# Kernel optimization log

Measured on AMD Instinct MI355X. Metric: run time of the kernel, lower is better.

The kernel has to match this reference:

```python
import jax, jax.numpy as jnp
import numpy as np

TRUNK = 128  # hard-coded trunk_size in the Triton kernels


def setup_inputs() -> dict:
    key = jax.random.key(0)
    kq, kk, kv = jax.random.split(key, 3)
    N, D = 262144, 64
    Q = jax.random.normal(kq, (N, D), dtype=jnp.float32)
    K = jax.random.normal(kk, (N, D), dtype=jnp.float32)
    V = jax.random.normal(kv, (N, D), dtype=jnp.float32)
    return {"Q": Q, "K": K, "V": V}


def reference(Q, K, V):
    # Faithful to the Triton module:
    # 1) intra kernel overwrites Q in-place with, per trunk t:
    #      Q_t <- Q_t @ (V_t^T K_t)^T = Q_t @ K_t^T @ V_t
    # 2) inter kernel accumulates global state S = sum_t V_t^T K_t = V^T K (fp32)
    # 3) final output = Q_intra @ S
    N, D = Q.shape
    dtype = Q.dtype
    assert N % TRUNK == 0
    T = N // TRUNK
    Qt = Q.reshape(T, TRUNK, D)
    Kt = K.reshape(T, TRUNK, D)
    Vt = V.reshape(T, TRUNK, D)
    # per-trunk scores [T, TRUNK, TRUNK], then apply to V
    scores = jnp.einsum('tnd,tmd->tnm', Qt, Kt)
    Q_intra = jnp.einsum('tnm,tmd->tnd', scores, Vt).reshape(N, D)
    # global DxD state in float32 (atomic_add accumulator dtype)
    S = jnp.einsum('nd,ne->de', V.astype(jnp.float32), K.astype(jnp.float32))
    out = Q_intra @ S.astype(dtype)
    return out
```

## Files before the change

kernel.cpp:

```cpp
#include <hip/hip_runtime.h>
#include <hip/hip_bf16.h>


#define TRUNK 128
#define DD 64
#define NPART 512

typedef __bf16 bf16x8 __attribute__((ext_vector_type(8)));
typedef float  f32x4  __attribute__((ext_vector_type(4)));
typedef unsigned int   u32;
typedef unsigned short u16;
typedef u32 u32x4 __attribute__((ext_vector_type(4)));
typedef u32 u32x2 __attribute__((ext_vector_type(2)));

union F8 { bf16x8 v; u16 u[8]; u32x4 q; };

__device__ __forceinline__ u16 f2bf(float x) {
    union { float f; u32 u; } a; a.f = x;
    u32 u = a.u;
    return (u16)((u + 0x7FFFu + ((u >> 16) & 1u)) >> 16);
}
__device__ __forceinline__ u32 pack2(float a, float b) {
    return (u32)f2bf(a) | ((u32)f2bf(b) << 16);
}

#define P_S  72
#define KV_T 136

__device__ __forceinline__ void stage_T(const float* __restrict__ M, long tb,
                                        u16* __restrict__ MT, int t) {
    #pragma unroll
    for (int i = 0; i < 2; ++i) {
        int pid = i * 256 + t;
        int rr = (pid >> 4) * 4;
        int c  = (pid & 15) * 4;
        float4 r0 = *(const float4*)(M + tb + (rr + 0) * 64 + c);
        float4 r1 = *(const float4*)(M + tb + (rr + 1) * 64 + c);
        float4 r2 = *(const float4*)(M + tb + (rr + 2) * 64 + c);
        float4 r3 = *(const float4*)(M + tb + (rr + 3) * 64 + c);
        const float* p0 = (const float*)&r0; const float* p1 = (const float*)&r1;
        const float* p2 = (const float*)&r2; const float* p3 = (const float*)&r3;
        #pragma unroll
        for (int j = 0; j < 4; ++j) {
            u32x2 w; w[0] = pack2(p0[j], p1[j]); w[1] = pack2(p2[j], p3[j]);
            *(u32x2*)&MT[(c + j) * KV_T + rr] = w;
        }
    }
}

__global__ __launch_bounds__(256) void s_partial(const float* __restrict__ K,
                                                 const float* __restrict__ V,
                                                 float* __restrict__ P) {
    __shared__ __align__(16) u16 lds[2 * 64 * KV_T];
    u16* KT = lds;
    u16* VT = lds + 64 * KV_T;

    const int t    = threadIdx.x;
    const int lane = t & 63;
    const int wave = t >> 6;
    const int l15  = lane & 15;
    const int quad = lane >> 4;
    const int mt0  = (wave >> 1) << 1;
    const int nt0  = (wave & 1) << 1;

    f32x4 gacc[2][2] = {};
    const long rowbase = (long)blockIdx.x * 512;

    for (int c = 0; c < 4; ++c) {
        const long tb = (rowbase + c * 128) * 64;
        stage_T(K, tb, KT, t);
        stage_T(V, tb, VT, t);
        __syncthreads();
        #pragma unroll
        for (int kt = 0; kt < 4; ++kt) {
            const int rbase = kt * 32 + quad * 8;
            F8 af[2], bf[2];
            #pragma unroll
            for (int mi = 0; mi < 2; ++mi)
                af[mi].q = *(const u32x4*)&VT[((mt0 + mi) * 16 + l15) * KV_T + rbase];
            #pragma unroll
            for (int ni = 0; ni < 2; ++ni)
                bf[ni].q = *(const u32x4*)&KT[((nt0 + ni) * 16 + l15) * KV_T + rbase];
            #pragma unroll
            for (int mi = 0; mi < 2; ++mi)
                #pragma unroll
                for (int ni = 0; ni < 2; ++ni)
                    gacc[mi][ni] = __builtin_amdgcn_mfma_f32_16x16x32_bf16(
                        af[mi].v, bf[ni].v, gacc[mi][ni], 0, 0, 0);
        }
        __syncthreads();
    }

    float* o = P + (long)blockIdx.x * 4096;
    #pragma unroll
    for (int mi = 0; mi < 2; ++mi)
        #pragma unroll
        for (int ni = 0; ni < 2; ++ni) {
            const int b0 = (mt0 + mi) * 16 + quad * 4;
            const int a  = (nt0 + ni) * 16 + l15;
            const float* g = (const float*)&gacc[mi][ni];
            #pragma unroll
            for (int reg = 0; reg < 4; ++reg)
                o[(b0 + reg) * 64 + a] = g[reg];
        }
}

__global__ __launch_bounds__(256) void s_reduce(const float* __restrict__ P,
                                                float* __restrict__ S) {
    const int tid = blockIdx.x * 256 + threadIdx.x;
    const int eg  = tid & 1023;
    const int way = tid >> 10;
    const float4* p = (const float4*)P;
    float4 acc = {0.f, 0.f, 0.f, 0.f};
    #pragma unroll 4
    for (int i = 0; i < 64; ++i) {
        float4 v = p[(long)(way * 64 + i) * 1024 + eg];
        acc.x += v.x; acc.y += v.y; acc.z += v.z; acc.w += v.w;
    }
    atomicAdd(&S[eg * 4 + 0], acc.x);
    atomicAdd(&S[eg * 4 + 1], acc.y);
    atomicAdd(&S[eg * 4 + 2], acc.z);
    atomicAdd(&S[eg * 4 + 3], acc.w);
}

#define KT_OFF 0
#define VT_OFF (64 * KV_T)
#define ST_OFF (2 * 64 * KV_T)
#define LDS_ELEMS (2 * 64 * KV_T + 64 * P_S)

__global__ __launch_bounds__(256, 3) void trunk_kernel(const float* __restrict__ Q,
                                                       const float* __restrict__ K,
                                                       const float* __restrict__ V,
                                                       const float* __restrict__ S,
                                                       float* __restrict__ out) {
    __shared__ __align__(16) u16 lds[LDS_ELEMS];
    u16* KT  = lds + KT_OFF;
    u16* VT  = lds + VT_OFF;
    u16* STb = lds + ST_OFF;
    u16* Gb  = lds + KT_OFF;
    u16* HTb = lds + VT_OFF;

    const int t    = threadIdx.x;
    const int lane = t & 63;
    const int wave = t >> 6;
    const int l15  = lane & 15;
    const int quad = lane >> 4;
    const long tb  = (long)blockIdx.x * (TRUNK * DD);

    F8 a3[2][2];
    #pragma unroll
    for (int kt = 0; kt < 2; ++kt)
        #pragma unroll
        for (int mi = 0; mi < 2; ++mi) {
            const int r = (wave * 2 + mi) * 16 + l15;
            const float* qp = Q + tb + r * 64 + kt * 32 + quad * 8;
            float4 q0 = *(const float4*)qp;
            float4 q1 = *(const float4*)(qp + 4);
            a3[kt][mi].q[0] = pack2(q0.x, q0.y);
            a3[kt][mi].q[1] = pack2(q0.z, q0.w);
            a3[kt][mi].q[2] = pack2(q1.x, q1.y);
            a3[kt][mi].q[3] = pack2(q1.z, q1.w);
        }

    stage_T(K, tb, KT, t);
    stage_T(V, tb, VT, t);
    #pragma unroll
    for (int i = 0; i < 4; ++i) {
        int f4 = i * 256 + t;
        int b = f4 >> 4, c = (f4 & 15) << 2;
        float4 s4 = ((const float4*)S)[f4];
        const float* sp = (const float*)&s4;
        #pragma unroll
        for (int j = 0; j < 4; ++j) STb[(c + j) * P_S + b] = f2bf(sp[j]);
    }
    __syncthreads();

    const int mt0 = (wave >> 1) << 1;
    const int nt0 = (wave & 1) << 1;
    f32x4 gacc[2][2] = {};
    #pragma unroll
    for (int kt = 0; kt < 4; ++kt) {
        const int rbase = kt * 32 + quad * 8;
        F8 af[2], bf[2];
        #pragma unroll
        for (int mi = 0; mi < 2; ++mi)
            af[mi].q = *(const u32x4*)&VT[((mt0 + mi) * 16 + l15) * KV_T + rbase];
        #pragma unroll
        for (int ni = 0; ni < 2; ++ni)
            bf[ni].q = *(const u32x4*)&KT[((nt0 + ni) * 16 + l15) * KV_T + rbase];
        #pragma unroll
        for (int mi = 0; mi < 2; ++mi)
            #pragma unroll
            for (int ni = 0; ni < 2; ++ni)
                gacc[mi][ni] = __builtin_amdgcn_mfma_f32_16x16x32_bf16(
                    af[mi].v, bf[ni].v, gacc[mi][ni], 0, 0, 0);
    }
    __syncthreads();

    #pragma unroll
    for (int mi = 0; mi < 2; ++mi)
        #pragma unroll
        for (int ni = 0; ni < 2; ++ni) {
            const int ga  = (nt0 + ni) * 16 + l15;
            const int gb0 = (mt0 + mi) * 16 + quad * 4;
            const float* g = (const float*)&gacc[mi][ni];
            u32x2 w; w[0] = pack2(g[0], g[1]); w[1] = pack2(g[2], g[3]);
            *(u32x2*)&Gb[ga * P_S + gb0] = w;
        }
    __syncthreads();

    f32x4 hacc[2][2] = {};
    #pragma unroll
    for (int kt = 0; kt < 2; ++kt) {
        const int kb = kt * 32 + quad * 8;
        F8 a2[2], b2[2];
        #pragma unroll
        for (int mi = 0; mi < 2; ++mi)
            a2[mi].q = *(const u32x4*)&Gb[((mt0 + mi) * 16 + l15) * P_S + kb];
        #pragma unroll
        for (int ni = 0; ni < 2; ++ni)
            b2[ni].q = *(const u32x4*)&STb[((nt0 + ni) * 16 + l15) * P_S + kb];
        #pragma unroll
        for (int mi = 0; mi < 2; ++mi)
            #pragma unroll
            for (int ni = 0; ni < 2; ++ni)
                hacc[mi][ni] = __builtin_amdgcn_mfma_f32_16x16x32_bf16(
                    a2[mi].v, b2[ni].v, hacc[mi][ni], 0, 0, 0);
    }
    #pragma unroll
    for (int mi = 0; mi < 2; ++mi)
        #pragma unroll
        for (int ni = 0; ni < 2; ++ni) {
            const int hc  = (nt0 + ni) * 16 + l15;
            const int ha0 = (mt0 + mi) * 16 + quad * 4;
            const float* h = (const float*)&hacc[mi][ni];
            u32x2 w; w[0] = pack2(h[0], h[1]); w[1] = pack2(h[2], h[3]);
            *(u32x2*)&HTb[hc * P_S + ha0] = w;
        }
    __syncthreads();

    f32x4 oacc[2][4] = {};
    #pragma unroll
    for (int kt = 0; kt < 2; ++kt) {
        const int ka = kt * 32 + quad * 8;
        #pragma unroll
        for (int ni = 0; ni < 4; ++ni) {
            F8 bb;
            bb.q = *(const u32x4*)&HTb[(ni * 16 + l15) * P_S + ka];
            #pragma unroll
            for (int mi = 0; mi < 2; ++mi)
                oacc[mi][ni] = __builtin_amdgcn_mfma_f32_16x16x32_bf16(
                    a3[kt][mi].v, bb.v, oacc[mi][ni], 0, 0, 0);
        }
    }
    #pragma unroll
    for (int mi = 0; mi < 2; ++mi)
        #pragma unroll
        for (int ni = 0; ni < 4; ++ni) {
            const int row0 = (wave * 2 + mi) * 16 + quad * 4;
            const int col  = ni * 16 + l15;
            const float* o = (const float*)&oacc[mi][ni];
            #pragma unroll
            for (int reg = 0; reg < 4; ++reg)
                out[tb + (long)(row0 + reg) * 64 + col] = o[reg];
        }
}

extern "C" void kernel_launch(void* const* d_in, const int* in_sizes, int n_in,
                              void* d_out, int out_size, void* d_ws, size_t ws_size,
                              hipStream_t stream) {
    const float* Q = (const float*)d_in[0];
    const float* K = (const float*)d_in[1];
    const float* V = (const float*)d_in[2];
    float* out = (float*)d_out;
    float* S   = (float*)d_ws;

    const int n = in_sizes[0] / DD;
    float* P = out + ((long)out_size - (long)NPART * 4096);

    hipMemsetAsync(S, 0, DD * DD * sizeof(float), stream);
    s_partial<<<NPART, 256, 0, stream>>>(K, V, P);
    s_reduce<<<32, 256, 0, stream>>>(P, S);
    trunk_kernel<<<n / TRUNK, 256, 0, stream>>>(Q, K, V, S, out);
}
```

Measured before the change: 239.2 us.

## Widen transposed LDS staging, double S-partial blocks, widen reduce grid

Staging K and V into transposed bf16 LDS tiles now has each thread read 8 rows and issue one 16-byte LDS write per column, replacing the old 8-byte writes. The S tile staging in trunk_kernel uses the same pattern. s_partial now covers 256 rows per block across 1024 blocks with an occupancy hint of 4, and s_reduce runs 256 blocks with fewer items each to expose more parallelism. The trade-off is more partial buffers, more atomics and possible LDS bank conflicts from the new write pattern.

After: 246.9 us. +3.2%, slower.

```diff
diff --git a/kernel.cpp b/kernel.cpp
--- a/kernel.cpp
+++ b/kernel.cpp
@@ -4,7 +4,7 @@
 
 #define TRUNK 128
 #define DD 64
-#define NPART 512
+#define NPART 1024
 
 typedef __bf16 bf16x8 __attribute__((ext_vector_type(8)));
 typedef float  f32x4  __attribute__((ext_vector_type(4)));
@@ -27,30 +27,28 @@
 #define P_S  72
 #define KV_T 136
 
-__device__ __forceinline__ void stage_T(const float* __restrict__ M, long tb,
-                                        u16* __restrict__ MT, int t) {
-    #pragma unroll
-    for (int i = 0; i < 2; ++i) {
-        int pid = i * 256 + t;
-        int rr = (pid >> 4) * 4;
-        int c  = (pid & 15) * 4;
-        float4 r0 = *(const float4*)(M + tb + (rr + 0) * 64 + c);
-        float4 r1 = *(const float4*)(M + tb + (rr + 1) * 64 + c);
-        float4 r2 = *(const float4*)(M + tb + (rr + 2) * 64 + c);
-        float4 r3 = *(const float4*)(M + tb + (rr + 3) * 64 + c);
-        const float* p0 = (const float*)&r0; const float* p1 = (const float*)&r1;
-        const float* p2 = (const float*)&r2; const float* p3 = (const float*)&r3;
-        #pragma unroll
-        for (int j = 0; j < 4; ++j) {
-            u32x2 w; w[0] = pack2(p0[j], p1[j]); w[1] = pack2(p2[j], p3[j]);
-            *(u32x2*)&MT[(c + j) * KV_T + rr] = w;
-        }
-    }
-}
-
-__global__ __launch_bounds__(256) void s_partial(const float* __restrict__ K,
-                                                 const float* __restrict__ V,
-                                                 float* __restrict__ P) {
+__device__ __forceinline__ void stage_T256(const float* __restrict__ M, long tb,
+                                           u16* __restrict__ MT, int t) {
+    const int c0 = (t >> 4) * 4;
+    const int r0 = (t & 15) * 8;
+    float4 rw[8];
+    #pragma unroll
+    for (int i = 0; i < 8; ++i)
+        rw[i] = *(const float4*)(M + tb + (long)(r0 + i) * 64 + c0);
+    #pragma unroll
+    for (int j = 0; j < 4; ++j) {
+        u32x4 w;
+        w[0] = pack2(((const float*)&rw[0])[j], ((const float*)&rw[1])[j]);
+        w[1] = pack2(((const float*)&rw[2])[j], ((const float*)&rw[3])[j]);
+        w[2] = pack2(((const float*)&rw[4])[j], ((const float*)&rw[5])[j]);
+        w[3] = pack2(((const float*)&rw[6])[j], ((const float*)&rw[7])[j]);
+        *(u32x4*)&MT[(c0 + j) * KV_T + r0] = w;
+    }
+}
+
+__global__ __launch_bounds__(256, 4) void s_partial(const float* __restrict__ K,
+                                                    const float* __restrict__ V,
+                                                    float* __restrict__ P) {
     __shared__ __align__(16) u16 lds[2 * 64 * KV_T];
     u16* KT = lds;
     u16* VT = lds + 64 * KV_T;
@@ -64,12 +62,12 @@
     const int nt0  = (wave & 1) << 1;
 
     f32x4 gacc[2][2] = {};
-    const long rowbase = (long)blockIdx.x * 512;
-
-    for (int c = 0; c < 4; ++c) {
+    const long rowbase = (long)blockIdx.x * 256;
+
+    for (int c = 0; c < 2; ++c) {
         const long tb = (rowbase + c * 128) * 64;
-        stage_T(K, tb, KT, t);
-        stage_T(V, tb, VT, t);
+        stage_T256(K, tb, KT, t);
+        stage_T256(V, tb, VT, t);
         __syncthreads();
         #pragma unroll
         for (int kt = 0; kt < 4; ++kt) {
@@ -113,8 +111,8 @@
     const float4* p = (const float4*)P;
     float4 acc = {0.f, 0.f, 0.f, 0.f};
     #pragma unroll 4
-    for (int i = 0; i < 64; ++i) {
-        float4 v = p[(long)(way * 64 + i) * 1024 + eg];
+    for (int i = 0; i < 16; ++i) {
+        float4 v = p[(long)(way * 16 + i) * 1024 + eg];
         acc.x += v.x; acc.y += v.y; acc.z += v.z; acc.w += v.w;
     }
     atomicAdd(&S[eg * 4 + 0], acc.x);
@@ -162,16 +160,25 @@
             a3[kt][mi].q[3] = pack2(q1.z, q1.w);
         }
 
-    stage_T(K, tb, KT, t);
-    stage_T(V, tb, VT, t);
-    #pragma unroll
-    for (int i = 0; i < 4; ++i) {
-        int f4 = i * 256 + t;
-        int b = f4 >> 4, c = (f4 & 15) << 2;
-        float4 s4 = ((const float4*)S)[f4];
-        const float* sp = (const float*)&s4;
-        #pragma unroll
-        for (int j = 0; j < 4; ++j) STb[(c + j) * P_S + b] = f2bf(sp[j]);
+    stage_T256(K, tb, KT, t);
+    stage_T256(V, tb, VT, t);
+
+    {
+        const int sb0 = (t & 7) * 8;
+        const int sc0 = (t >> 3) * 2;
+        float2 sv[8];
+        #pragma unroll
+        for (int i = 0; i < 8; ++i)
+            sv[i] = *(const float2*)(S + (sb0 + i) * 64 + sc0);
+        #pragma unroll
+        for (int j = 0; j < 2; ++j) {
+            u32x4 w;
+            w[0] = pack2(((const float*)&sv[0])[j], ((const float*)&sv[1])[j]);
+            w[1] = pack2(((const float*)&sv[2])[j], ((const float*)&sv[3])[j]);
+            w[2] = pack2(((const float*)&sv[4])[j], ((const float*)&sv[5])[j]);
+            w[3] = pack2(((const float*)&sv[6])[j], ((const float*)&sv[7])[j]);
+            *(u32x4*)&STb[(sc0 + j) * P_S + sb0] = w;
+        }
     }
     __syncthreads();
 
@@ -280,6 +287,6 @@
 
     hipMemsetAsync(S, 0, DD * DD * sizeof(float), stream);
     s_partial<<<NPART, 256, 0, stream>>>(K, V, P);
-    s_reduce<<<32, 256, 0, stream>>>(P, S);
+    s_reduce<<<256, 256, 0, stream>>>(P, S);
     trunk_kernel<<<n / TRUNK, 256, 0, stream>>>(Q, K, V, S, out);
 }
```
